# Optimization experiments

Measured on AMD Instinct MI355X. Metric: run time of the kernel, lower is better.

The kernel has to match this reference:

```python
import jax, jax.numpy as jnp
import numpy as np

B, N, E_PER, DIN, DOUT = 64, 1024, 16384, 128, 128
NN, E = B * N, B * E_PER
K = int(0.5 * N)  # TopKPooling ratio=0.5, fixed per-graph node count
EPS_BN = 1e-5


def setup_inputs():
    key = jax.random.key(0)
    ks = jax.random.split(key, 16)
    x = jax.random.normal(ks[0], (NN, DIN), jnp.float32)
    # edges constrained within each graph (offset + local index)
    offs = jnp.repeat(jnp.arange(B, dtype=jnp.int32) * N, E_PER)
    src = offs + jax.random.randint(ks[1], (E,), 0, N, dtype=jnp.int32)
    dst = offs + jax.random.randint(ks[2], (E,), 0, N, dtype=jnp.int32)
    edge_index = jnp.stack([src, dst])  # [2, E]
    edge_attr = jax.random.normal(ks[3], (E, DIN), jnp.float32)
    batch_idx = jnp.repeat(jnp.arange(B, dtype=jnp.int32), N)
    s = 1.0 / np.sqrt(DIN)
    Wq = jax.random.normal(ks[4], (DIN, DOUT), jnp.float32) * s
    bq = jnp.zeros((DOUT,), jnp.float32)
    Wk = jax.random.normal(ks[5], (DIN, DOUT), jnp.float32) * s
    bk = jnp.zeros((DOUT,), jnp.float32)
    Wv = jax.random.normal(ks[6], (DIN, DOUT), jnp.float32) * s
    bv = jnp.zeros((DOUT,), jnp.float32)
    We = jax.random.normal(ks[7], (DIN, DOUT), jnp.float32) * s
    be = jnp.zeros((DOUT,), jnp.float32)
    Ws = jax.random.normal(ks[8], (DIN, DOUT), jnp.float32) * s  # root/skip weight
    bs = jnp.zeros((DOUT,), jnp.float32)
    pool_w = jax.random.normal(ks[9], (DOUT,), jnp.float32)
    gamma = jnp.ones((DOUT,), jnp.float32)
    beta = jnp.zeros((DOUT,), jnp.float32)
    return {"x": x, "edge_index": edge_index, "edge_attr": edge_attr,
            "batch_idx": batch_idx, "Wq": Wq, "bq": bq, "Wk": Wk, "bk": bk,
            "Wv": Wv, "bv": bv, "We": We, "be": be, "Ws": Ws, "bs": bs,
            "pool_w": pool_w, "gamma": gamma, "beta": beta}


def reference(x, edge_index, edge_attr, batch_idx, Wq, bq, Wk, bk, Wv, bv,
              We, be, Ws, bs, pool_w, gamma, beta):
    src, dst = edge_index[0], edge_index[1]
    # ---- TransformerConv (heads=1, concat) ----
    q = x @ Wq + bq                      # [NN, D]
    k = x @ Wk + bk
    v = x @ Wv + bv
    e = edge_attr @ We + be              # [E, D]
    ke = k[src] + e
    alpha = jnp.sum(q[dst] * ke, axis=-1) / jnp.sqrt(jnp.float32(DOUT))  # [E]
    # segment softmax over incoming edges of each dst node
    m = jax.ops.segment_max(alpha, dst, num_segments=NN)
    ex = jnp.exp(alpha - m[dst])
    denom = jax.ops.segment_sum(ex, dst, num_segments=NN)
    attn = ex / (denom[dst] + 1e-16)
    msg = attn[:, None] * (v[src] + e)   # [E, D]
    out = jax.ops.segment_sum(msg, dst, num_segments=NN)
    out = out + (x @ Ws + bs)            # root weight (skip)
    out = jax.nn.relu(out)
    # ---- TopKPooling ----
    score = jnp.tanh(out @ pool_w / jnp.linalg.norm(pool_w))  # [NN]
    top_s, top_i = jax.lax.top_k(score.reshape(B, N), K)      # [B, K]
    offs = (jnp.arange(B, dtype=top_i.dtype) * N)[:, None]
    perm = (top_i + offs).reshape(-1)                          # [B*K] global ids
    xp = out[perm] * top_s.reshape(-1)[:, None]                # [B*K, D]
    batch_out = jnp.repeat(jnp.arange(B, dtype=jnp.int32), K)
    # remap / filter edges: keep edges with both endpoints kept
    node_map = jnp.full((NN,), -1, dtype=jnp.int32).at[perm].set(
        jnp.arange(B * K, dtype=jnp.int32))
    ns, nd = node_map[src], node_map[dst]
    valid = (ns >= 0) & (nd >= 0)                              # [E] edge mask
    new_edge_index = jnp.where(valid[None, :], jnp.stack([ns, nd]), -1)
    new_edge_attr = edge_attr * valid[:, None].astype(edge_attr.dtype)
    # ---- BatchNorm1d (training: batch stats, biased variance) ----
    mu = jnp.mean(xp, axis=0)
    var = jnp.mean(jnp.square(xp - mu), axis=0)
    y = gamma * (xp - mu) * jax.lax.rsqrt(var + EPS_BN) + beta
    return (y, new_edge_index, new_edge_attr, batch_out, valid)
```

## Files before the change

### kernel.cpp

```cpp
#include <hip/hip_runtime.h>
#include <cstddef>
#include <cstdint>

#define NODES 65536
#define NEDGE 1048576
#define NB    64
#define NPER  1024
#define TOPK  512
#define BKR   32768
#define DIM   128
#define NM    ((size_t)NODES * DIM)

typedef float f32x4 __attribute__((ext_vector_type(4)));

__device__ __forceinline__ f32x4 ntload4(const f32x4* p) {
  return __builtin_nontemporal_load(p);
}
__device__ __forceinline__ void ntstore4(f32x4* p, f32x4 v) {
  __builtin_nontemporal_store(v, p);
}
__device__ __forceinline__ long long ntloadll(const long long* p) {
  return __builtin_nontemporal_load(p);
}
__device__ __forceinline__ float dotv(f32x4 a, f32x4 b) {
  return fmaf(a.x, b.x, fmaf(a.y, b.y, fmaf(a.z, b.z, a.w * b.w)));
}

__device__ __forceinline__ void gemm_core(
    const float* __restrict__ A, const f32x4* __restrict__ sW,
    const float* __restrict__ bias, float* __restrict__ Out,
    size_t row0, int ostride, int tc) {
  const float* a0 = A + row0 * 128;
  f32x4 acc0[8], acc1[8];
#pragma unroll
  for (int r = 0; r < 8; ++r) { acc0[r] = (f32x4)(0.f); acc1[r] = (f32x4)(0.f); }
#pragma unroll 4
  for (int k4 = 0; k4 < 32; ++k4) {
    f32x4 a[8];
#pragma unroll
    for (int r = 0; r < 8; ++r)
      a[r] = *reinterpret_cast<const f32x4*>(a0 + r * 128 + k4 * 4);
#pragma unroll
    for (int kk = 0; kk < 4; ++kk) {
      const f32x4 w0 = sW[(k4 * 4 + kk) * 32 + tc * 2];
      const f32x4 w1 = sW[(k4 * 4 + kk) * 32 + tc * 2 + 1];
#pragma unroll
      for (int r = 0; r < 8; ++r) {
        const float av = a[r][kk];
        acc0[r] += av * w0;
        acc1[r] += av * w1;
      }
    }
  }
  const f32x4 b0 = reinterpret_cast<const f32x4*>(bias)[tc * 2];
  const f32x4 b1 = reinterpret_cast<const f32x4*>(bias)[tc * 2 + 1];
#pragma unroll
  for (int r = 0; r < 8; ++r) {
    f32x4* outp = reinterpret_cast<f32x4*>(Out + (row0 + r) * (size_t)ostride + tc * 8);
    outp[0] = acc0[r] + b0;
    outp[1] = acc1[r] + b1;
  }
}

__global__ __launch_bounds__(512) void gemm_multi(
    const float* __restrict__ x,
    const float* __restrict__ Wq, const float* __restrict__ bq, float* __restrict__ q,
    const float* __restrict__ Wk, const float* __restrict__ bk,
    const float* __restrict__ Wv, const float* __restrict__ bv, float* __restrict__ kv,
    const float* __restrict__ Ws, const float* __restrict__ bs, float* __restrict__ sl,
    const float* __restrict__ Wc, const float* __restrict__ bc, float* __restrict__ qw) {
  __shared__ f32x4 sW[128 * 32];
  const int which = blockIdx.x >> 8;
  const int bid = blockIdx.x & 255;
  const int t = threadIdx.x;
  const float* W; const float* bias; float* Out; int ostride = 128;
  if (which == 0)      { W = Wq; bias = bq; Out = q; }
  else if (which == 1) { W = Wk; bias = bk; Out = kv;       ostride = 256; }
  else if (which == 2) { W = Wv; bias = bv; Out = kv + 128; ostride = 256; }
  else if (which == 3) { W = Ws; bias = bs; Out = sl; }
  else                 { W = Wc; bias = bc; Out = qw; }
  const f32x4* W4 = reinterpret_cast<const f32x4*>(W);
#pragma unroll
  for (int i = 0; i < 8; ++i) sW[t + i * 512] = W4[t + i * 512];
  __syncthreads();
  gemm_core(x, sW, bias, Out, (size_t)bid * 256 + (t >> 4) * 8, ostride, t & 15);
}

__global__ __launch_bounds__(256) void gemm_final(
    const float* __restrict__ A, const float* __restrict__ W,
    const float* __restrict__ bias, const float* __restrict__ aggv,
    const float* __restrict__ sl, const float* __restrict__ pwn,
    float* __restrict__ outc, float* __restrict__ score) {
  __shared__ f32x4 sW[128 * 32];
  const int t = threadIdx.x;
  const f32x4* W4 = reinterpret_cast<const f32x4*>(W);
#pragma unroll
  for (int i = 0; i < 16; ++i) sW[t + i * 256] = W4[t + i * 256];
  const int tc = t & 15;
  const size_t row0 = (size_t)blockIdx.x * 128 + (t >> 4) * 8;
  const float* a0 = A + row0 * 128;
  f32x4 acc0[8], acc1[8];
#pragma unroll
  for (int r = 0; r < 8; ++r) { acc0[r] = (f32x4)(0.f); acc1[r] = (f32x4)(0.f); }
  __syncthreads();
#pragma unroll 4
  for (int k4 = 0; k4 < 32; ++k4) {
    f32x4 a[8];
#pragma unroll
    for (int r = 0; r < 8; ++r)
      a[r] = *reinterpret_cast<const f32x4*>(a0 + r * 128 + k4 * 4);
#pragma unroll
    for (int kk = 0; kk < 4; ++kk) {
      const f32x4 w0 = sW[(k4 * 4 + kk) * 32 + tc * 2];
      const f32x4 w1 = sW[(k4 * 4 + kk) * 32 + tc * 2 + 1];
#pragma unroll
      for (int r = 0; r < 8; ++r) {
        const float av = a[r][kk];
        acc0[r] += av * w0;
        acc1[r] += av * w1;
      }
    }
  }
  const f32x4 b0 = reinterpret_cast<const f32x4*>(bias)[tc * 2];
  const f32x4 b1 = reinterpret_cast<const f32x4*>(bias)[tc * 2 + 1];
  const f32x4 p0 = reinterpret_cast<const f32x4*>(pwn)[tc * 2];
  const f32x4 p1 = reinterpret_cast<const f32x4*>(pwn)[tc * 2 + 1];
#pragma unroll
  for (int r = 0; r < 8; ++r) {
    const f32x4 v0 = reinterpret_cast<const f32x4*>(aggv + (row0 + r) * 128 + tc * 8)[0];
    const f32x4 v1 = reinterpret_cast<const f32x4*>(aggv + (row0 + r) * 128 + tc * 8)[1];
    const f32x4 s0 = reinterpret_cast<const f32x4*>(sl + (row0 + r) * 128 + tc * 8)[0];
    const f32x4 s1 = reinterpret_cast<const f32x4*>(sl + (row0 + r) * 128 + tc * 8)[1];
    f32x4 o0 = acc0[r] + b0 + v0 + s0;
    f32x4 o1 = acc1[r] + b1 + v1 + s1;
#pragma unroll
    for (int c = 0; c < 4; ++c) { o0[c] = fmaxf(o0[c], 0.f); o1[c] = fmaxf(o1[c], 0.f); }
    f32x4* outp = reinterpret_cast<f32x4*>(outc + (row0 + r) * 128 + tc * 8);
    outp[0] = o0; outp[1] = o1;
    float sp = dotv(o0, p0) + dotv(o1, p1);
#pragma unroll
    for (int d = 1; d < 16; d <<= 1) sp += __shfl_xor(sp, d, 16);
    if (tc == 0) score[row0 + r] = tanhf(sp);
  }
}

__global__ void wc_kernel(const float* __restrict__ Wq, const float* __restrict__ bq,
                          const float* __restrict__ We, float* __restrict__ Wc,
                          float* __restrict__ bc) {
  __shared__ float sWe[128];
  const int i = blockIdx.x;
  const int t = threadIdx.x;
  sWe[t] = We[i * 128 + t];
  __syncthreads();
  float s = 0.f;
  for (int d = 0; d < 128; ++d) s = fmaf(Wq[t * 128 + d], sWe[d], s);
  Wc[t * 128 + i] = s;
  if (t == 0) {
    float sb = 0.f;
    for (int d = 0; d < 128; ++d) sb = fmaf(bq[d], sWe[d], sb);
    bc[i] = sb;
  }
}

__global__ void init_kernel(int* __restrict__ deg, int* __restrict__ nmap,
                            float* __restrict__ bn2) {
  const int i = blockIdx.x * 256 + threadIdx.x;
  if (i < NODES) { deg[i] = 0; nmap[i] = -1; }
  if (i < 256) bn2[i] = 0.f;
}

__global__ void pwn_kernel(const float* __restrict__ pool_w, float* __restrict__ pwn) {
  __shared__ float red[128];
  const int t = threadIdx.x;
  const float vv = pool_w[t];
  red[t] = vv * vv;
  __syncthreads();
  for (int d = 64; d > 0; d >>= 1) {
    if (t < d) red[t] += red[t + d];
    __syncthreads();
  }
  pwn[t] = vv * rsqrtf(red[0]);
}

__global__ void deg_kernel(const int* __restrict__ dst, int* __restrict__ deg) {
  const int e = blockIdx.x * 256 + threadIdx.x;
  atomicAdd(&deg[dst[e]], 1);
}

__global__ __launch_bounds__(1024) void scan_kernel(const int* __restrict__ deg,
                                                    int* __restrict__ offs,
                                                    int* __restrict__ woff) {
  __shared__ int part[1024];
  const int t = threadIdx.x;
  const int base = t * 64;
  int s = 0;
  for (int j = 0; j < 64; ++j) s += deg[base + j];
  part[t] = s;
  __syncthreads();
  for (int d = 1; d < 1024; d <<= 1) {
    const int add = (t >= d) ? part[t - d] : 0;
    __syncthreads();
    part[t] += add;
    __syncthreads();
  }
  int run = part[t] - s;
  for (int j = 0; j < 64; ++j) {
    offs[base + j] = run; woff[base + j] = run;
    run += deg[base + j];
  }
  if (t == 1023) offs[NODES] = run;
}

__global__ void scatter_kernel(const int* __restrict__ dst, const int* __restrict__ src,
                               int* __restrict__ woff, long long* __restrict__ srt) {
  const int e = blockIdx.x * 256 + threadIdx.x;
  const int pos = atomicAdd(&woff[dst[e]], 1);
  srt[pos] = ((long long)src[e] << 32) | (unsigned)e;
}

__global__ __launch_bounds__(256) void attn_v4(
    const float* __restrict__ q, const float* __restrict__ kv,
    const float* __restrict__ qw, const float* __restrict__ ea,
    const float* __restrict__ be, const long long* __restrict__ srt,
    const int* __restrict__ offs, float* __restrict__ aggv,
    float* __restrict__ agge) {
  int b = blockIdx.x;
  b = (b & 7) * 2048 + (b >> 3);
  const int wid = b * 4 + (threadIdx.x >> 6);
  const int lane = threadIdx.x & 63;
  const int g = lane >> 4;
  const int l = lane & 15;
  const f32x4* q4  = reinterpret_cast<const f32x4*>(q)  + (size_t)wid * 32;
  const f32x4* qw4 = reinterpret_cast<const f32x4*>(qw) + (size_t)wid * 32;
  const f32x4* be4 = reinterpret_cast<const f32x4*>(be);
  const f32x4 qv0 = q4[2 * l],  qv1 = q4[2 * l + 1];
  const f32x4 qwv0 = qw4[2 * l], qwv1 = qw4[2 * l + 1];
  float qbe = dotv(qv0, be4[2 * l]) + dotv(qv1, be4[2 * l + 1]);
#pragma unroll
  for (int d = 1; d < 16; d <<= 1) qbe += __shfl_xor(qbe, d, 64);

  const f32x4* kv4 = reinterpret_cast<const f32x4*>(kv);
  const f32x4* ea4 = reinterpret_cast<const f32x4*>(ea);
  float denom = 0.f;
  f32x4 av0 = (f32x4)(0.f), av1 = (f32x4)(0.f), ag0 = (f32x4)(0.f), ag1 = (f32x4)(0.f);
  const int e0 = offs[wid], e1 = offs[wid + 1];
  for (int p = e0 + g; p < e1; p += 8) {
    const bool h2 = (p + 4) < e1;
    const long long pkA = ntloadll(srt + p);
    const long long pkB = h2 ? ntloadll(srt + p + 4) : pkA;
    const int eA = (int)pkA, sA = (int)(pkA >> 32);
    const int eB = (int)pkB, sB = (int)(pkB >> 32);
    const f32x4* kvA = kv4 + (size_t)sA * 64 + 2 * l;
    const f32x4* kvB = kv4 + (size_t)sB * 64 + 2 * l;
    const f32x4 kA0 = kvA[0], kA1 = kvA[1], vA0 = kvA[32], vA1 = kvA[33];
    const f32x4 kB0 = kvB[0], kB1 = kvB[1], vB0 = kvB[32], vB1 = kvB[33];
    const f32x4 fA0 = ntload4(ea4 + (size_t)eA * 32 + 2 * l);
    const f32x4 fA1 = ntload4(ea4 + (size_t)eA * 32 + 2 * l + 1);
    const f32x4 fB0 = ntload4(ea4 + (size_t)eB * 32 + 2 * l);
    const f32x4 fB1 = ntload4(ea4 + (size_t)eB * 32 + 2 * l + 1);
    float pA = dotv(qv0, kA0) + dotv(qv1, kA1) + dotv(qwv0, fA0) + dotv(qwv1, fA1);
    float pB = dotv(qv0, kB0) + dotv(qv1, kB1) + dotv(qwv0, fB0) + dotv(qwv1, fB1);
#pragma unroll
    for (int d = 1; d < 16; d <<= 1) {
      pA += __shfl_xor(pA, d, 64);
      pB += __shfl_xor(pB, d, 64);
    }
    const float wA = expf((pA + qbe) * 0.08838834764831845f);
    const float wB = h2 ? expf((pB + qbe) * 0.08838834764831845f) : 0.f;
    denom += wA + wB;
    av0 += wA * vA0 + wB * vB0;
    av1 += wA * vA1 + wB * vB1;
    ag0 += wA * fA0 + wB * fB0;
    ag1 += wA * fA1 + wB * fB1;
  }
#pragma unroll
  for (int d = 16; d < 64; d <<= 1) {
    denom += __shfl_xor(denom, d, 64);
#pragma unroll
    for (int c = 0; c < 4; ++c) {
      av0[c] += __shfl_xor(av0[c], d, 64);
      av1[c] += __shfl_xor(av1[c], d, 64);
      ag0[c] += __shfl_xor(ag0[c], d, 64);
      ag1[c] += __shfl_xor(ag1[c], d, 64);
    }
  }
  if (g == 0) {
    const float inv = 1.f / (denom + 1e-16f);
    f32x4* aggv4 = reinterpret_cast<f32x4*>(aggv) + (size_t)wid * 32;
    f32x4* agge4 = reinterpret_cast<f32x4*>(agge) + (size_t)wid * 32;
    aggv4[2 * l]     = av0 * inv;
    aggv4[2 * l + 1] = av1 * inv;
    agge4[2 * l]     = ag0 * inv;
    agge4[2 * l + 1] = ag1 * inv;
  }
}

__global__ __launch_bounds__(1024) void topk_kernel(
    const float* __restrict__ score, int* __restrict__ perm,
    float* __restrict__ tops, float* __restrict__ batchf, int* __restrict__ nmap) {
  __shared__ float ss[1024];
  __shared__ int si[1024];
  const int b = blockIdx.x, t = threadIdx.x;
  ss[t] = score[b * 1024 + t];
  si[t] = t;
  __syncthreads();
  for (int size = 2; size <= 1024; size <<= 1) {
    for (int stride = size >> 1; stride > 0; stride >>= 1) {
      const int j = t ^ stride;
      if (j > t) {
        const float s1 = ss[t], s2 = ss[j];
        const int i1 = si[t], i2 = si[j];
        const bool bj = (s2 > s1) || (s2 == s1 && i2 < i1);
        const bool dir = ((t & size) == 0);
        if (dir ? bj : !bj) { ss[t] = s2; ss[j] = s1; si[t] = i2; si[j] = i1; }
      }
      __syncthreads();
    }
  }
  if (t < TOPK) {
    const int g = b * TOPK + t;
    perm[g] = b * 1024 + si[t];
    tops[g] = ss[t];
    batchf[g] = (float)b;
    nmap[b * 1024 + si[t]] = g;
  }
}

__global__ __launch_bounds__(128) void xp_kernel(
    const float* __restrict__ outc, const int* __restrict__ perm,
    const float* __restrict__ tops, float* __restrict__ y,
    float* __restrict__ bnsum, float* __restrict__ bnsq) {
  const int t = threadIdx.x;
  const int r0 = blockIdx.x * 128;
  float s = 0.f, s2 = 0.f;
  for (int i = 0; i < 128; ++i) {
    const int r = r0 + i;
    const int g = perm[r];
    const float val = outc[(size_t)g * DIM + t] * tops[r];
    y[(size_t)r * DIM + t] = val;
    s += val;
    s2 = fmaf(val, val, s2);
  }
  atomicAdd(&bnsum[t], s);
  atomicAdd(&bnsq[t], s2);
}

__global__ __launch_bounds__(256) void bnapply_v2(
    float* __restrict__ y, const float* __restrict__ bnsum, const float* __restrict__ bnsq,
    const float* __restrict__ gamma, const float* __restrict__ beta) {
  const size_t i4 = (size_t)blockIdx.x * 256 + threadIdx.x;
  const int c4 = (int)(i4 & 31);
  f32x4 a, c;
#pragma unroll
  for (int j = 0; j < 4; ++j) {
    const int col = c4 * 4 + j;
    const float mu = bnsum[col] * (1.f / BKR);
    const float var = bnsq[col] * (1.f / BKR) - mu * mu;
    const float aa = gamma[col] * rsqrtf(var + 1e-5f);
    a[j] = aa;
    c[j] = beta[col] - mu * aa;
  }
  f32x4 v = reinterpret_cast<f32x4*>(y)[i4];
#pragma unroll
  for (int j = 0; j < 4; ++j) v[j] = fmaf(v[j], a[j], c[j]);
  reinterpret_cast<f32x4*>(y)[i4] = v;
}

__global__ __launch_bounds__(256) void efnea_kernel(
    const int* __restrict__ srcArr, const int* __restrict__ dstArr,
    const int* __restrict__ nm, const float* __restrict__ ea,
    float* __restrict__ nei, float* __restrict__ validf, float* __restrict__ nea) {
  const int row = blockIdx.x * 8 + (threadIdx.x >> 5);
  const int lane = threadIdx.x & 31;
  const int ns = nm[srcArr[row]];
  const int nd = nm[dstArr[row]];
  const bool val = (ns >= 0) && (nd >= 0);
  if (lane == 0) {
    nei[row] = val ? (float)ns : -1.f;
    nei[NEDGE + row] = val ? (float)nd : -1.f;
    validf[row] = val ? 1.f : 0.f;
  }
  const size_t i4 = (size_t)row * 32 + lane;
  f32x4 v = (f32x4)(0.f);
  if (val) v = ntload4(reinterpret_cast<const f32x4*>(ea) + i4);
  ntstore4(reinterpret_cast<f32x4*>(nea) + i4, v);
}

extern "C" void kernel_launch(void* const* d_in, const int* in_sizes, int n_in,
                              void* d_out, int out_size, void* d_ws, size_t ws_size,
                              hipStream_t stream) {
  const float* x     = (const float*)d_in[0];
  const int*   eidx  = (const int*)d_in[1];
  const float* eattr = (const float*)d_in[2];
  const float* Wq = (const float*)d_in[4];  const float* bq = (const float*)d_in[5];
  const float* Wk = (const float*)d_in[6];  const float* bk = (const float*)d_in[7];
  const float* Wv = (const float*)d_in[8];  const float* bv = (const float*)d_in[9];
  const float* We = (const float*)d_in[10]; const float* be = (const float*)d_in[11];
  const float* Ws = (const float*)d_in[12]; const float* bs = (const float*)d_in[13];
  const float* pool_w = (const float*)d_in[14];
  const float* gamma  = (const float*)d_in[15];
  const float* beta   = (const float*)d_in[16];

  const int* srcArr = eidx;
  const int* dstArr = eidx + NEDGE;

  float* out = (float*)d_out;
  float* y      = out;
  float* nei    = out + (size_t)BKR * DIM;
  float* nea    = nei + 2 * (size_t)NEDGE;
  float* batchf = nea + (size_t)NEDGE * DIM;
  float* validf = batchf + BKR;

  float* q    = nea + 0 * NM;
  float* kv   = nea + 1 * NM;
  float* sl   = nea + 3 * NM;
  float* qw   = nea + 4 * NM;
  float* aggv = nea + 5 * NM;
  float* agge = nea + 6 * NM;
  float* outc = nea + 7 * NM;

  char* w = (char*)d_ws;
  size_t off = 0;
  float* score= (float*)(w + off); off += (size_t)NODES * 4;
  float* pwn  = (float*)(w + off); off += 128 * 4;
  float* Wc   = (float*)(w + off); off += 128 * 128 * 4;
  float* bc   = (float*)(w + off); off += 128 * 4;
  float* tops = (float*)(w + off); off += (size_t)BKR * 4;
  float* bnsum= (float*)(w + off); off += 128 * 4;
  float* bnsq = (float*)(w + off); off += 128 * 4;
  int* deg    = (int*)(w + off); off += (size_t)NODES * 4;
  int* offs   = (int*)(w + off); off += ((size_t)NODES + 8) * 4;
  int* woff   = (int*)(w + off); off += (size_t)NODES * 4;
  int* nmap   = (int*)(w + off); off += (size_t)NODES * 4;
  int* perm   = (int*)(w + off); off += (size_t)BKR * 4;
  long long* srt = (long long*)(w + off); off += (size_t)NEDGE * 8;

  init_kernel<<<NODES / 256, 256, 0, stream>>>(deg, nmap, bnsum);
  pwn_kernel<<<1, 128, 0, stream>>>(pool_w, pwn);
  wc_kernel<<<128, 128, 0, stream>>>(Wq, bq, We, Wc, bc);

  gemm_multi<<<5 * 256, 512, 0, stream>>>(
      x, Wq, bq, q, Wk, bk, Wv, bv, kv, Ws, bs, sl, Wc, bc, qw);

  deg_kernel<<<NEDGE / 256, 256, 0, stream>>>(dstArr, deg);
  scan_kernel<<<1, 1024, 0, stream>>>(deg, offs, woff);
  scatter_kernel<<<NEDGE / 256, 256, 0, stream>>>(dstArr, srcArr, woff, srt);

  attn_v4<<<NODES / 4, 256, 0, stream>>>(q, kv, qw, eattr, be, srt, offs, aggv, agge);

  gemm_final<<<NODES / 128, 256, 0, stream>>>(agge, We, be, aggv, sl, pwn, outc, score);

  topk_kernel<<<NB, 1024, 0, stream>>>(score, perm, tops, batchf, nmap);

  xp_kernel<<<BKR / 128, 128, 0, stream>>>(outc, perm, tops, y, bnsum, bnsq);
  bnapply_v2<<<(BKR * 32) / 256, 256, 0, stream>>>(y, bnsum, bnsq, gamma, beta);

  efnea_kernel<<<NEDGE / 8, 256, 0, stream>>>(srcArr, dstArr, nmap, eattr, nei, validf, nea);
}
```

Before: 735.3 us.

## Fuse skip GEMM into final GEMM, merge setup kernels, use fast exp

The root/skip projection x@Ws is no longer computed in gemm_multi and written to an intermediate buffer. The final GEMM now accumulates it in a second phase that reloads shared weights. This removes one 32 MB intermediate write and its later read, at the cost of re-reading x in the final kernel. The three small init, pool-norm and Wc kernels are merged into one launch, and the attention softmax uses __expf, which is less precise than expf.

Measured after the change: 731.2 us. Within noise of the previous version (-0.6%).

```diff
diff --git a/kernel.cpp b/kernel.cpp
--- a/kernel.cpp
+++ b/kernel.cpp
@@ -67,7 +67,6 @@
     const float* __restrict__ Wq, const float* __restrict__ bq, float* __restrict__ q,
     const float* __restrict__ Wk, const float* __restrict__ bk,
     const float* __restrict__ Wv, const float* __restrict__ bv, float* __restrict__ kv,
-    const float* __restrict__ Ws, const float* __restrict__ bs, float* __restrict__ sl,
     const float* __restrict__ Wc, const float* __restrict__ bc, float* __restrict__ qw) {
   __shared__ f32x4 sW[128 * 32];
   const int which = blockIdx.x >> 8;
@@ -77,7 +76,6 @@
   if (which == 0)      { W = Wq; bias = bq; Out = q; }
   else if (which == 1) { W = Wk; bias = bk; Out = kv;       ostride = 256; }
   else if (which == 2) { W = Wv; bias = bv; Out = kv + 128; ostride = 256; }
-  else if (which == 3) { W = Ws; bias = bs; Out = sl; }
   else                 { W = Wc; bias = bc; Out = qw; }
   const f32x4* W4 = reinterpret_cast<const f32x4*>(W);
 #pragma unroll
@@ -86,53 +84,61 @@
   gemm_core(x, sW, bias, Out, (size_t)bid * 256 + (t >> 4) * 8, ostride, t & 15);
 }
 
-__global__ __launch_bounds__(256) void gemm_final(
-    const float* __restrict__ A, const float* __restrict__ W,
-    const float* __restrict__ bias, const float* __restrict__ aggv,
-    const float* __restrict__ sl, const float* __restrict__ pwn,
+__global__ __launch_bounds__(256) void gemm_final2(
+    const float* __restrict__ agge, const float* __restrict__ We,
+    const float* __restrict__ x,    const float* __restrict__ Ws,
+    const float* __restrict__ be,   const float* __restrict__ bs,
+    const float* __restrict__ aggv, const float* __restrict__ pwn,
     float* __restrict__ outc, float* __restrict__ score) {
   __shared__ f32x4 sW[128 * 32];
   const int t = threadIdx.x;
-  const f32x4* W4 = reinterpret_cast<const f32x4*>(W);
-#pragma unroll
-  for (int i = 0; i < 16; ++i) sW[t + i * 256] = W4[t + i * 256];
   const int tc = t & 15;
   const size_t row0 = (size_t)blockIdx.x * 128 + (t >> 4) * 8;
-  const float* a0 = A + row0 * 128;
   f32x4 acc0[8], acc1[8];
 #pragma unroll
   for (int r = 0; r < 8; ++r) { acc0[r] = (f32x4)(0.f); acc1[r] = (f32x4)(0.f); }
-  __syncthreads();
+
+#pragma unroll
+  for (int phase = 0; phase < 2; ++phase) {
+    const float* W = phase ? Ws : We;
+    const float* A = phase ? x : agge;
+    const f32x4* W4 = reinterpret_cast<const f32x4*>(W);
+    if (phase) __syncthreads();
+#pragma unroll
+    for (int i = 0; i < 16; ++i) sW[t + i * 256] = W4[t + i * 256];
+    __syncthreads();
+    const float* a0 = A + row0 * 128;
 #pragma unroll 4
-  for (int k4 = 0; k4 < 32; ++k4) {
-    f32x4 a[8];
-#pragma unroll
-    for (int r = 0; r < 8; ++r)
-      a[r] = *reinterpret_cast<const f32x4*>(a0 + r * 128 + k4 * 4);
-#pragma unroll
-    for (int kk = 0; kk < 4; ++kk) {
-      const f32x4 w0 = sW[(k4 * 4 + kk) * 32 + tc * 2];
-      const f32x4 w1 = sW[(k4 * 4 + kk) * 32 + tc * 2 + 1];
-#pragma unroll
-      for (int r = 0; r < 8; ++r) {
-        const float av = a[r][kk];
-        acc0[r] += av * w0;
-        acc1[r] += av * w1;
+    for (int k4 = 0; k4 < 32; ++k4) {
+      f32x4 a[8];
+#pragma unroll
+      for (int r = 0; r < 8; ++r)
+        a[r] = *reinterpret_cast<const f32x4*>(a0 + r * 128 + k4 * 4);
+#pragma unroll
+      for (int kk = 0; kk < 4; ++kk) {
+        const f32x4 w0 = sW[(k4 * 4 + kk) * 32 + tc * 2];
+        const f32x4 w1 = sW[(k4 * 4 + kk) * 32 + tc * 2 + 1];
+#pragma unroll
+        for (int r = 0; r < 8; ++r) {
+          const float av = a[r][kk];
+          acc0[r] += av * w0;
+          acc1[r] += av * w1;
+        }
       }
     }
   }
-  const f32x4 b0 = reinterpret_cast<const f32x4*>(bias)[tc * 2];
-  const f32x4 b1 = reinterpret_cast<const f32x4*>(bias)[tc * 2 + 1];
+  const f32x4 b0 = reinterpret_cast<const f32x4*>(be)[tc * 2] +
+                   reinterpret_cast<const f32x4*>(bs)[tc * 2];
+  const f32x4 b1 = reinterpret_cast<const f32x4*>(be)[tc * 2 + 1] +
+                   reinterpret_cast<const f32x4*>(bs)[tc * 2 + 1];
   const f32x4 p0 = reinterpret_cast<const f32x4*>(pwn)[tc * 2];
   const f32x4 p1 = reinterpret_cast<const f32x4*>(pwn)[tc * 2 + 1];
 #pragma unroll
   for (int r = 0; r < 8; ++r) {
     const f32x4 v0 = reinterpret_cast<const f32x4*>(aggv + (row0 + r) * 128 + tc * 8)[0];
     const f32x4 v1 = reinterpret_cast<const f32x4*>(aggv + (row0 + r) * 128 + tc * 8)[1];
-    const f32x4 s0 = reinterpret_cast<const f32x4*>(sl + (row0 + r) * 128 + tc * 8)[0];
-    const f32x4 s1 = reinterpret_cast<const f32x4*>(sl + (row0 + r) * 128 + tc * 8)[1];
-    f32x4 o0 = acc0[r] + b0 + v0 + s0;
-    f32x4 o1 = acc1[r] + b1 + v1 + s1;
+    f32x4 o0 = acc0[r] + b0 + v0;
+    f32x4 o1 = acc1[r] + b1 + v1;
 #pragma unroll
     for (int c = 0; c < 4; ++c) { o0[c] = fmaxf(o0[c], 0.f); o1[c] = fmaxf(o1[c], 0.f); }
     f32x4* outp = reinterpret_cast<f32x4*>(outc + (row0 + r) * 128 + tc * 8);
@@ -144,42 +150,44 @@
   }
 }
 
-__global__ void wc_kernel(const float* __restrict__ Wq, const float* __restrict__ bq,
-                          const float* __restrict__ We, float* __restrict__ Wc,
-                          float* __restrict__ bc) {
-  __shared__ float sWe[128];
-  const int i = blockIdx.x;
+__global__ __launch_bounds__(256) void setup_kernel(
+    const float* __restrict__ pool_w, float* __restrict__ pwn,
+    const float* __restrict__ Wq, const float* __restrict__ bq,
+    const float* __restrict__ We, float* __restrict__ Wc, float* __restrict__ bc,
+    int* __restrict__ deg, int* __restrict__ nmap, float* __restrict__ bn2) {
+  const int blk = blockIdx.x;
   const int t = threadIdx.x;
-  sWe[t] = We[i * 128 + t];
-  __syncthreads();
-  float s = 0.f;
-  for (int d = 0; d < 128; ++d) s = fmaf(Wq[t * 128 + d], sWe[d], s);
-  Wc[t * 128 + i] = s;
-  if (t == 0) {
-    float sb = 0.f;
-    for (int d = 0; d < 128; ++d) sb = fmaf(bq[d], sWe[d], sb);
-    bc[i] = sb;
-  }
-}
-
-__global__ void init_kernel(int* __restrict__ deg, int* __restrict__ nmap,
-                            float* __restrict__ bn2) {
-  const int i = blockIdx.x * 256 + threadIdx.x;
-  if (i < NODES) { deg[i] = 0; nmap[i] = -1; }
-  if (i < 256) bn2[i] = 0.f;
-}
-
-__global__ void pwn_kernel(const float* __restrict__ pool_w, float* __restrict__ pwn) {
-  __shared__ float red[128];
-  const int t = threadIdx.x;
-  const float vv = pool_w[t];
-  red[t] = vv * vv;
-  __syncthreads();
-  for (int d = 64; d > 0; d >>= 1) {
-    if (t < d) red[t] += red[t + d];
+  if (blk < 256) {
+    const int i = blk * 256 + t;
+    deg[i] = 0; nmap[i] = -1;
+    if (i < 256) bn2[i] = 0.f;
+  } else if (blk == 256) {
+    __shared__ float red[128];
+    if (t < 128) {
+      const float vv = pool_w[t];
+      red[t] = vv * vv;
+    }
     __syncthreads();
-  }
-  pwn[t] = vv * rsqrtf(red[0]);
+    for (int d = 64; d > 0; d >>= 1) {
+      if (t < d) red[t] += red[t + d];
+      __syncthreads();
+    }
+    if (t < 128) pwn[t] = pool_w[t] * rsqrtf(red[0]);
+  } else {
+    __shared__ float sWe[2][128];
+    const int i = (blk - 257) * 2 + (t >> 7);
+    const int tl = t & 127;
+    sWe[t >> 7][tl] = We[i * 128 + tl];
+    __syncthreads();
+    float s = 0.f;
+    for (int d = 0; d < 128; ++d) s = fmaf(Wq[tl * 128 + d], sWe[t >> 7][d], s);
+    Wc[tl * 128 + i] = s;
+    if (tl == 0) {
+      float sb = 0.f;
+      for (int d = 0; d < 128; ++d) sb = fmaf(bq[d], sWe[t >> 7][d], sb);
+      bc[i] = sb;
+    }
+  }
 }
 
 __global__ void deg_kernel(const int* __restrict__ dst, int* __restrict__ deg) {
@@ -218,7 +226,7 @@
   srt[pos] = ((long long)src[e] << 32) | (unsigned)e;
 }
 
-__global__ __launch_bounds__(256) void attn_v4(
+__global__ __launch_bounds__(256) void attn_v6(
     const float* __restrict__ q, const float* __restrict__ kv,
     const float* __restrict__ qw, const float* __restrict__ ea,
     const float* __restrict__ be, const long long* __restrict__ srt,
@@ -265,8 +273,8 @@
       pA += __shfl_xor(pA, d, 64);
       pB += __shfl_xor(pB, d, 64);
     }
-    const float wA = expf((pA + qbe) * 0.08838834764831845f);
-    const float wB = h2 ? expf((pB + qbe) * 0.08838834764831845f) : 0.f;
+    const float wA = __expf((pA + qbe) * 0.08838834764831845f);
+    const float wB = h2 ? __expf((pB + qbe) * 0.08838834764831845f) : 0.f;
     denom += wA + wB;
     av0 += wA * vA0 + wB * vB0;
     av1 += wA * vA1 + wB * vB1;
@@ -413,11 +421,10 @@
 
   float* q    = nea + 0 * NM;
   float* kv   = nea + 1 * NM;
-  float* sl   = nea + 3 * NM;
-  float* qw   = nea + 4 * NM;
-  float* aggv = nea + 5 * NM;
-  float* agge = nea + 6 * NM;
-  float* outc = nea + 7 * NM;
+  float* qw   = nea + 3 * NM;
+  float* aggv = nea + 4 * NM;
+  float* agge = nea + 5 * NM;
+  float* outc = nea + 6 * NM;
 
   char* w = (char*)d_ws;
   size_t off = 0;
@@ -435,20 +442,20 @@
   int* perm   = (int*)(w + off); off += (size_t)BKR * 4;
   long long* srt = (long long*)(w + off); off += (size_t)NEDGE * 8;
 
-  init_kernel<<<NODES / 256, 256, 0, stream>>>(deg, nmap, bnsum);
-  pwn_kernel<<<1, 128, 0, stream>>>(pool_w, pwn);
-  wc_kernel<<<128, 128, 0, stream>>>(Wq, bq, We, Wc, bc);
-
-  gemm_multi<<<5 * 256, 512, 0, stream>>>(
-      x, Wq, bq, q, Wk, bk, Wv, bv, kv, Ws, bs, sl, Wc, bc, qw);
+  setup_kernel<<<321, 256, 0, stream>>>(pool_w, pwn, Wq, bq, We, Wc, bc,
+                                        deg, nmap, (float*)bnsum);
+
+  gemm_multi<<<4 * 256, 512, 0, stream>>>(
+      x, Wq, bq, q, Wk, bk, Wv, bv, kv, Wc, bc, qw);
 
   deg_kernel<<<NEDGE / 256, 256, 0, stream>>>(dstArr, deg);
   scan_kernel<<<1, 1024, 0, stream>>>(deg, offs, woff);
   scatter_kernel<<<NEDGE / 256, 256, 0, stream>>>(dstArr, srcArr, woff, srt);
 
-  attn_v4<<<NODES / 4, 256, 0, stream>>>(q, kv, qw, eattr, be, srt, offs, aggv, agge);
-
-  gemm_final<<<NODES / 128, 256, 0, stream>>>(agge, We, be, aggv, sl, pwn, outc, score);
+  attn_v6<<<NODES / 4, 256, 0, stream>>>(q, kv, qw, eattr, be, srt, offs, aggv, agge);
+
+  gemm_final2<<<NODES / 128, 256, 0, stream>>>(agge, We, x, Ws, be, bs, aggv, pwn,
+                                               outc, score);
 
   topk_kernel<<<NB, 1024, 0, stream>>>(score, perm, tops, batchf, nmap);
 
```
